# Optimization experiments

Hardware: AMD Instinct MI355X
Metric: run time of the kernel (lower is better)

Reference implementation:

```python
import jax, jax.numpy as jnp
import numpy as np

TEMPERATURE = 0.07
NEG_INF = -1e9


def setup_inputs() -> dict:
    key = jax.random.key(0)
    k1, k2, k3, k4, k5 = jax.random.split(key, 5)
    B, L, H = 64, 256, 64
    query_embs = jax.random.normal(k1, (B, L, H), dtype=jnp.float32)
    key_embs = jax.random.normal(k2, (B, L, H), dtype=jnp.float32)
    labels = jax.random.randint(k3, (B,), 0, 2, dtype=jnp.int64)
    q_mask = jax.random.randint(k4, (B, L), 0, 2, dtype=jnp.int32)
    k_mask = jax.random.randint(k5, (B, L), 0, 2, dtype=jnp.int32)
    return {"query_embs": query_embs, "key_embs": key_embs, "labels": labels,
            "q_mask": q_mask, "k_mask": k_mask}


def reference(query_embs, key_embs, labels, q_mask, k_mask):
    # ColBERT-style late interaction over all B x B pairs.
    # sim: (B_q, B_k, Lq, Lk) token-level dot products.
    sim = jnp.einsum('bqh,ckh->bcqk', query_embs, key_embs)
    # Mask out padded key tokens before the max over key positions.
    sim = jnp.where(k_mask[None, :, None, :].astype(bool), sim, NEG_INF)
    maxsim = jnp.max(sim, axis=-1)                      # (B_q, B_k, Lq)
    qm = q_mask[:, None, :].astype(maxsim.dtype)        # (B_q, 1, Lq)
    scores = jnp.sum(maxsim * qm, axis=-1) / TEMPERATURE  # (B_q, B_k)
    # Cross-entropy on rows with labels==1, target = diagonal index.
    logp = jax.nn.log_softmax(scores, axis=-1)
    B = scores.shape[0]
    diag = logp[jnp.arange(B), jnp.arange(B)]           # (B,)
    w = labels.astype(scores.dtype)
    denom = jnp.maximum(jnp.sum(w), 1.0)
    return -jnp.sum(w * diag) / denom
```

## Files before the change

kernel.cpp:

```cpp
#include <hip/hip_runtime.h>
#include <math.h>

#define PB 64
#define PL 256
#define PH 64
#define TEMP 0.07f
#define NEG_INF_F (-1e9f)

#define KFTILE 1024
#define KFSLAB (16 * KFTILE)
#define BGRP   8

typedef short short8 __attribute__((ext_vector_type(8)));
typedef float f32x4 __attribute__((ext_vector_type(4)));

__device__ __forceinline__ unsigned short f32_to_bf16(float f) {
    unsigned int u = __float_as_uint(f);
    u += 0x7FFFu + ((u >> 16) & 1u);
    return (unsigned short)(u >> 16);
}

__device__ __forceinline__ int frag_off(int p, int cc) {
    return ((p >> 4) * KFTILE) + ((cc >> 3) * 512) +
           (((((cc >> 1) & 3) * 16) + (p & 15)) * 8) + ((cc & 1) * 4);
}

__global__ __launch_bounds__(256)
void prep_kernel(const float* __restrict__ Q,
                 const float* __restrict__ K,
                 const int*   __restrict__ kmask,
                 const int*   __restrict__ qmask,
                 unsigned short* __restrict__ Qfrag,
                 unsigned short* __restrict__ Kfrag,
                 int* __restrict__ nvK,
                 int* __restrict__ nvQ) {
    const int tid  = threadIdx.x;
    const int lane = tid & 63;
    const int wave = tid >> 6;
    __shared__ int posArr[PL];
    __shared__ int wcnt[4];

    const bool isQ = (blockIdx.x >= 256);
    const int  bid = isQ ? (blockIdx.x - 256) : blockIdx.x;
    const int  idx     = bid >> 2;
    const int  quarter = bid & 3;

    const int* mask = isQ ? (qmask + idx * PL) : (kmask + idx * PL);
    const int km = mask[tid];
    unsigned long long bal = __ballot(km != 0);
    int within = __popcll(bal & ((1ull << lane) - 1ull));
    if (lane == 0) wcnt[wave] = __popcll(bal);
    __syncthreads();
    int base = 0;
    #pragma unroll
    for (int w = 0; w < 4; ++w) base += (w < wave) ? wcnt[w] : 0;
    posArr[tid] = km ? (base + within) : -1;
    const int nv = wcnt[0] + wcnt[1] + wcnt[2] + wcnt[3];
    __syncthreads();

    const int sub = lane >> 4;
    const int cl  = lane & 15;
    const float* src = (isQ ? Q : K) + (size_t)idx * PL * PH;
    unsigned short* slab = (isQ ? Qfrag : Kfrag) + (size_t)idx * KFSLAB;

    #pragma unroll
    for (int it = 0; it < 4; ++it) {
        int r = quarter * 64 + it * 16 + wave * 4 + sub;
        int p = posArr[r];
        if (p >= 0) {
            float4 v = *(const float4*)(src + (size_t)r * PH + cl * 4);
            ushort4 o;
            o.x = f32_to_bf16(v.x); o.y = f32_to_bf16(v.y);
            o.z = f32_to_bf16(v.z); o.w = f32_to_bf16(v.w);
            *(ushort4*)(slab + frag_off(p, cl)) = o;
        }
    }

    if (!isQ) {
        const int rows16 = (nv + 15) & ~15;
        const int padChunks = (rows16 - nv) * 16;
        if (tid < padChunks) {
            int row = nv + (tid >> 4);
            if (row >= quarter * 64 && row < quarter * 64 + 64)
                *(ushort4*)(slab + frag_off(row, tid & 15)) = (ushort4){0, 0, 0, 0};
        }
        if (quarter == 0 && tid == 0) nvK[idx] = nv;
    } else {
        #pragma unroll
        for (int it = 0; it < 4; ++it) {
            int id2 = it * 256 + tid;
            int row = quarter * 64 + (id2 >> 4);
            if (row >= nv)
                *(ushort4*)(slab + frag_off(row, id2 & 15)) = (ushort4){0, 0, 0, 0};
        }
        if (quarter == 0 && tid == 0) nvQ[idx] = nv;
    }
}

__global__ __launch_bounds__(256, 2)
void colbert_scores_mfma(const unsigned short* __restrict__ Qfrag,
                         const unsigned short* __restrict__ Kfrag,
                         const int*   __restrict__ nvK,
                         const int*   __restrict__ nvQ,
                         float*       __restrict__ scores) {
    const int c  = blockIdx.x;
    const int bg = blockIdx.y;
    const int tid  = threadIdx.x;
    const int wave = tid >> 6;
    const int lane = tid & 63;
    const int n    = lane & 15;

    const int nv   = nvK[c];
    const int nt16 = (nv + 15) >> 4;

    const unsigned short* kb = Kfrag + (size_t)c * KFSLAB + lane * 8;
    short8 kreg[16][2];
    #pragma unroll
    for (int ct = 0; ct < 16; ++ct) {
        if (ct < nt16) {
            kreg[ct][0] = *(const short8*)(kb + ct * KFTILE);
            kreg[ct][1] = *(const short8*)(kb + ct * KFTILE + 512);
        }
    }

    const f32x4 ZERO4 = (f32x4){0.f, 0.f, 0.f, 0.f};

    #pragma unroll 1
    for (int bo = 0; bo < 2; ++bo) {
        const int b  = bg * BGRP + wave * 2 + bo;
        const int nq = nvQ[b];
        const int nQP = (nq + 31) >> 5;
        const unsigned short* qslab = Qfrag + (size_t)b * KFSLAB + lane * 8;

        float partial = 0.0f;

        #pragma unroll 1
        for (int qp = 0; qp < nQP; ++qp) {
            const unsigned short* qbase = qslab + qp * 2 * KFTILE;
            short8 a00 = *(const short8*)(qbase);
            short8 a01 = *(const short8*)(qbase + 512);
            short8 a10 = *(const short8*)(qbase + 1024);
            short8 a11 = *(const short8*)(qbase + 1536);

            float maxv[2][4];
            #pragma unroll
            for (int t = 0; t < 2; ++t)
                #pragma unroll
                for (int r = 0; r < 4; ++r) maxv[t][r] = NEG_INF_F;

            #pragma unroll
            for (int ct = 0; ct < 16; ++ct) {
                if (ct < nt16) {
                    const float bv = (ct * 16 + n < nv) ? 0.0f : NEG_INF_F;
                    const f32x4 B4 = (f32x4){bv, bv, bv, bv};

                    f32x4 acc0 = __builtin_amdgcn_mfma_f32_16x16x32_bf16(a00, kreg[ct][0], B4, 0, 0, 0);
                    acc0 = __builtin_amdgcn_mfma_f32_16x16x32_bf16(a01, kreg[ct][1], acc0, 0, 0, 0);
                    f32x4 acc1 = __builtin_amdgcn_mfma_f32_16x16x32_bf16(a10, kreg[ct][0], B4, 0, 0, 0);
                    acc1 = __builtin_amdgcn_mfma_f32_16x16x32_bf16(a11, kreg[ct][1], acc1, 0, 0, 0);

                    #pragma unroll
                    for (int r = 0; r < 4; ++r) {
                        maxv[0][r] = fmaxf(maxv[0][r], acc0[r]);
                        maxv[1][r] = fmaxf(maxv[1][r], acc1[r]);
                    }
                }
            }

            #pragma unroll
            for (int t = 0; t < 2; ++t)
                #pragma unroll
                for (int r = 0; r < 4; ++r) {
                    float mv = maxv[t][r];
                    mv = fmaxf(mv, __shfl_xor(mv, 1, 16));
                    mv = fmaxf(mv, __shfl_xor(mv, 2, 16));
                    mv = fmaxf(mv, __shfl_xor(mv, 4, 16));
                    mv = fmaxf(mv, __shfl_xor(mv, 8, 16));
                    if (n == 0) partial += mv;
                }
        }

        partial += __shfl_xor(partial, 16, 64);
        partial += __shfl_xor(partial, 32, 64);
        if (lane == 0) scores[b * PB + c] = partial * (1.0f / TEMP);
    }
}

__global__ void finalize_kernel(const float* __restrict__ scores,
                                const int*   __restrict__ labels,
                                float*       __restrict__ out) {
    const int r = threadIdx.x;
    const float* row = scores + r * PB;
    float mx = NEG_INF_F;
    for (int j = 0; j < PB; ++j) mx = fmaxf(mx, row[j]);
    float se = 0.0f;
    for (int j = 0; j < PB; ++j) se += expf(row[j] - mx);
    float logp_diag = row[r] - mx - logf(se);
    float w = (float)labels[r];
    float wd = w * logp_diag;
    #pragma unroll
    for (int off = 32; off >= 1; off >>= 1) {
        wd += __shfl_xor(wd, off, 64);
        w  += __shfl_xor(w,  off, 64);
    }
    if (r == 0) out[0] = -wd / fmaxf(w, 1.0f);
}

extern "C" void kernel_launch(void* const* d_in, const int* in_sizes, int n_in,
                              void* d_out, int out_size, void* d_ws, size_t ws_size,
                              hipStream_t stream) {
    const float* Q      = (const float*)d_in[0];
    const float* K      = (const float*)d_in[1];
    const int*   labels = (const int*)d_in[2];
    const int*   qmask  = (const int*)d_in[3];
    const int*   kmask  = (const int*)d_in[4];
    float*       out    = (float*)d_out;

    char* ws = (char*)d_ws;
    float*          scores = (float*)ws;
    unsigned short* Qfrag  = (unsigned short*)(ws + 16 * 1024);
    unsigned short* Kfrag  = (unsigned short*)(ws + 16 * 1024 + 2 * 1024 * 1024);
    int*            nvK    = (int*)(ws + 16 * 1024 + 4 * 1024 * 1024);
    int*            nvQ    = nvK + 64;

    prep_kernel<<<512, 256, 0, stream>>>(Q, K, kmask, qmask, Qfrag, Kfrag, nvK, nvQ);

    dim3 grid(PB, PB / BGRP);
    colbert_scores_mfma<<<grid, 256, 0, stream>>>(Qfrag, Kfrag, nvK, nvQ, scores);
    finalize_kernel<<<1, 64, 0, stream>>>(scores, labels, out);
}
```

Before: 98.84 us.

## Give each wave one query batch and prefetch next Q fragment tile

Halves the batch group size so each wave handles a single query batch instead of two, doubling the grid along that axis and repeating the K register loads per block. Inside the query-pair loop, the next iteration's Q fragments are loaded before the MFMA work on the current ones, hiding global load latency. The cost is extra registers for the prefetched fragments and twice as many K slab loads across the grid.

```diff
diff --git a/kernel.cpp b/kernel.cpp
--- a/kernel.cpp
+++ b/kernel.cpp
@@ -9,7 +9,7 @@
 
 #define KFTILE 1024
 #define KFSLAB (16 * KFTILE)
-#define BGRP   8
+#define BGRP   4
 
 typedef short short8 __attribute__((ext_vector_type(8)));
 typedef float f32x4 __attribute__((ext_vector_type(4)));
@@ -123,67 +123,75 @@
         }
     }
 
-    const f32x4 ZERO4 = (f32x4){0.f, 0.f, 0.f, 0.f};
+    const int b  = bg * BGRP + wave;
+    const int nq = nvQ[b];
+    const int nQP = (nq + 31) >> 5;
+    const unsigned short* qslab = Qfrag + (size_t)b * KFSLAB + lane * 8;
+
+    short8 c00, c01, c10, c11;
+    if (nQP > 0) {
+        c00 = *(const short8*)(qslab);
+        c01 = *(const short8*)(qslab + 512);
+        c10 = *(const short8*)(qslab + 1024);
+        c11 = *(const short8*)(qslab + 1536);
+    }
+
+    float partial = 0.0f;
 
     #pragma unroll 1
-    for (int bo = 0; bo < 2; ++bo) {
-        const int b  = bg * BGRP + wave * 2 + bo;
-        const int nq = nvQ[b];
-        const int nQP = (nq + 31) >> 5;
-        const unsigned short* qslab = Qfrag + (size_t)b * KFSLAB + lane * 8;
-
-        float partial = 0.0f;
-
-        #pragma unroll 1
-        for (int qp = 0; qp < nQP; ++qp) {
-            const unsigned short* qbase = qslab + qp * 2 * KFTILE;
-            short8 a00 = *(const short8*)(qbase);
-            short8 a01 = *(const short8*)(qbase + 512);
-            short8 a10 = *(const short8*)(qbase + 1024);
-            short8 a11 = *(const short8*)(qbase + 1536);
-
-            float maxv[2][4];
+    for (int qp = 0; qp < nQP; ++qp) {
+        short8 p00, p01, p10, p11;
+        if (qp + 1 < nQP) {
+            const unsigned short* nb = qslab + (qp + 1) * 2 * KFTILE;
+            p00 = *(const short8*)(nb);
+            p01 = *(const short8*)(nb + 512);
+            p10 = *(const short8*)(nb + 1024);
+            p11 = *(const short8*)(nb + 1536);
+        }
+
+        float maxv[2][4];
+        #pragma unroll
+        for (int t = 0; t < 2; ++t)
             #pragma unroll
-            for (int t = 0; t < 2; ++t)
+            for (int r = 0; r < 4; ++r) maxv[t][r] = NEG_INF_F;
+
+        #pragma unroll
+        for (int ct = 0; ct < 16; ++ct) {
+            if (ct < nt16) {
+                const float bv = (ct * 16 + n < nv) ? 0.0f : NEG_INF_F;
+                const f32x4 B4 = (f32x4){bv, bv, bv, bv};
+
+                f32x4 acc0 = __builtin_amdgcn_mfma_f32_16x16x32_bf16(c00, kreg[ct][0], B4, 0, 0, 0);
+                acc0 = __builtin_amdgcn_mfma_f32_16x16x32_bf16(c01, kreg[ct][1], acc0, 0, 0, 0);
+                f32x4 acc1 = __builtin_amdgcn_mfma_f32_16x16x32_bf16(c10, kreg[ct][0], B4, 0, 0, 0);
+                acc1 = __builtin_amdgcn_mfma_f32_16x16x32_bf16(c11, kreg[ct][1], acc1, 0, 0, 0);
+
                 #pragma unroll
-                for (int r = 0; r < 4; ++r) maxv[t][r] = NEG_INF_F;
-
-            #pragma unroll
-            for (int ct = 0; ct < 16; ++ct) {
-                if (ct < nt16) {
-                    const float bv = (ct * 16 + n < nv) ? 0.0f : NEG_INF_F;
-                    const f32x4 B4 = (f32x4){bv, bv, bv, bv};
-
-                    f32x4 acc0 = __builtin_amdgcn_mfma_f32_16x16x32_bf16(a00, kreg[ct][0], B4, 0, 0, 0);
-                    acc0 = __builtin_amdgcn_mfma_f32_16x16x32_bf16(a01, kreg[ct][1], acc0, 0, 0, 0);
-                    f32x4 acc1 = __builtin_amdgcn_mfma_f32_16x16x32_bf16(a10, kreg[ct][0], B4, 0, 0, 0);
-                    acc1 = __builtin_amdgcn_mfma_f32_16x16x32_bf16(a11, kreg[ct][1], acc1, 0, 0, 0);
-
-                    #pragma unroll
-                    for (int r = 0; r < 4; ++r) {
-                        maxv[0][r] = fmaxf(maxv[0][r], acc0[r]);
-                        maxv[1][r] = fmaxf(maxv[1][r], acc1[r]);
-                    }
+                for (int r = 0; r < 4; ++r) {
+                    maxv[0][r] = fmaxf(maxv[0][r], acc0[r]);
+                    maxv[1][r] = fmaxf(maxv[1][r], acc1[r]);
                 }
             }
-
+        }
+
+        #pragma unroll
+        for (int t = 0; t < 2; ++t)
             #pragma unroll
-            for (int t = 0; t < 2; ++t)
-                #pragma unroll
-                for (int r = 0; r < 4; ++r) {
-                    float mv = maxv[t][r];
-                    mv = fmaxf(mv, __shfl_xor(mv, 1, 16));
-                    mv = fmaxf(mv, __shfl_xor(mv, 2, 16));
-                    mv = fmaxf(mv, __shfl_xor(mv, 4, 16));
-                    mv = fmaxf(mv, __shfl_xor(mv, 8, 16));
-                    if (n == 0) partial += mv;
-                }
-        }
-
-        partial += __shfl_xor(partial, 16, 64);
-        partial += __shfl_xor(partial, 32, 64);
-        if (lane == 0) scores[b * PB + c] = partial * (1.0f / TEMP);
-    }
+            for (int r = 0; r < 4; ++r) {
+                float mv = maxv[t][r];
+                mv = fmaxf(mv, __shfl_xor(mv, 1, 16));
+                mv = fmaxf(mv, __shfl_xor(mv, 2, 16));
+                mv = fmaxf(mv, __shfl_xor(mv, 4, 16));
+                mv = fmaxf(mv, __shfl_xor(mv, 8, 16));
+                if (n == 0) partial += mv;
+            }
+
+        c00 = p00; c01 = p01; c10 = p10; c11 = p11;
+    }
+
+    partial += __shfl_xor(partial, 16, 64);
+    partial += __shfl_xor(partial, 32, 64);
+    if (lane == 0) scores[b * PB + c] = partial * (1.0f / TEMP);
 }
 
 __global__ void finalize_kernel(const float* __restrict__ scores,
```

Result: no change. 99.98 us (+1.2%).
